# Optimization experiments

Measured on AMD Instinct MI355X. Metric: run time of the kernel, lower is better.

Reference implementation:

```python
import jax, jax.numpy as jnp
import numpy as np

B, N, FEAT, HID, OUT = 128, 64, 4, 256, 4
E = N * (N - 1)  # fully-connected graph, no self-loops


def _onehot_rel():
    # off-diagonal (recv, send) pairs, matching NRI's encode_onehot construction
    recv, send = np.where(~np.eye(N, dtype=bool))
    rel_rec = np.eye(N, dtype=np.float32)[recv]   # [E, N]
    rel_send = np.eye(N, dtype=np.float32)[send]  # [E, N]
    return jnp.asarray(rel_rec), jnp.asarray(rel_send)


def setup_inputs() -> dict:
    key = jax.random.key(0)
    ks = jax.random.split(key, 8)
    rel_rec, rel_send = _onehot_rel()

    def xavier(k, shape):
        fan_in, fan_out = shape
        lim = (6.0 / (fan_in + fan_out)) ** 0.5
        return jax.random.uniform(k, shape, jnp.float32, -lim, lim)

    return {
        "inputs": jax.random.normal(ks[0], (B, N, FEAT), jnp.float32),
        "edges": jax.random.normal(ks[1], (B, E, 2), jnp.float32),  # unused by forward (as in source)
        "rel_rec": rel_rec,
        "rel_send": rel_send,
        "W_msg1": xavier(ks[2], (2 * FEAT, HID)), "b_msg1": jnp.zeros((HID,), jnp.float32),
        "W_msg2": xavier(ks[3], (HID, HID)),      "b_msg2": jnp.zeros((HID,), jnp.float32),
        "W_out1": xavier(ks[4], (FEAT + HID, HID)), "b_out1": jnp.zeros((HID,), jnp.float32),
        "W_out2": xavier(ks[5], (HID, HID)),      "b_out2": jnp.zeros((HID,), jnp.float32),
        "W_out3": xavier(ks[6], (HID, OUT)),      "b_out3": jnp.zeros((OUT,), jnp.float32),
    }


def reference(inputs, edges, rel_rec, rel_send,
              W_msg1, b_msg1, W_msg2, b_msg2,
              W_out1, b_out1, W_out2, b_out2, W_out3, b_out3):
    x = inputs.reshape(inputs.shape[0], inputs.shape[1], -1)  # [B, N, F]
    # gather node features to edges via one-hot matmuls (faithful to source)
    receivers = jnp.einsum('en,bnf->bef', rel_rec, x)   # [B, E, F]
    senders = jnp.einsum('en,bnf->bef', rel_send, x)    # [B, E, F]
    pre_msg = jnp.concatenate([receivers, senders], axis=-1)  # [B, E, 2F]
    # edge MLP (dropout_prob = 0.0 -> identity)
    msg = jax.nn.relu(pre_msg @ W_msg1 + b_msg1)
    msg = jax.nn.relu(msg @ W_msg2 + b_msg2)            # [B, E, HID]
    # scatter-aggregate back to nodes via rel_rec^T
    agg_msg = jnp.einsum('en,beh->bnh', rel_rec, msg)   # [B, N, HID]
    out = jnp.concatenate([x, agg_msg], axis=-1)        # [B, N, F+HID]
    out = jax.nn.relu(out @ W_out1 + b_out1)
    out = jax.nn.relu(out @ W_out2 + b_out2)
    out = out @ W_out3 + b_out3                          # [B, N, 4]
    return out
```

## Files before the change

kernel.cpp:

```cpp
#include <hip/hip_runtime.h>
#include <cstddef>

typedef _Float16 f16_t;
typedef _Float16 f16x8 __attribute__((ext_vector_type(8)));
typedef float    f32x4 __attribute__((ext_vector_type(4)));

static constexpr int NN = 64;
static constexpr int FF = 4;
static constexpr int HH = 256;


__device__ inline void pack_frag(const float* __restrict__ src, f16_t* __restrict__ dst,
                                 int fid, int ksteps, int mode)
{
    if (fid >= ksteps * 1024) return;
    int lane = fid & 63;
    int nt   = (fid >> 6) & 15;
    int ks   = fid >> 10;
    int col  = nt * 16 + (lane & 15);
    int kb   = ks * 32 + (lane >> 4) * 8;
    #pragma unroll
    for (int j = 0; j < 8; ++j) {
        int k = kb + j;
        float v;
        if (mode == 0) {
            v = src[k * 256 + col];
        } else {
            if (k < 256)      v = src[(4 + k) * 256 + col];
            else if (k < 260) v = src[(k - 256) * 256 + col];
            else              v = 0.f;
        }
        dst[(size_t)fid * 8 + j] = (f16_t)v;
    }
}

__global__ void prep_all(const float* __restrict__ x,
                         const float* __restrict__ W_msg1,
                         const float* __restrict__ W_msg2,
                         const float* __restrict__ W_out1,
                         const float* __restrict__ W_out2,
                         f16_t* __restrict__ W2p, f16_t* __restrict__ W1op,
                         f16_t* __restrict__ W2op, f16_t* __restrict__ Vp)
{
    int bid = blockIdx.x, tid = threadIdx.x;
    if (bid < 32) {
        pack_frag(W_msg2, W2p, bid * 256 + tid, 8, 0);
    } else if (bid < 68) {
        pack_frag(W_out1, W1op, (bid - 32) * 256 + tid, 9, 1);
    } else if (bid < 100) {
        pack_frag(W_out2, W2op, (bid - 68) * 256 + tid, 8, 0);
    } else {
        int gid  = (bid - 100) * 256 + tid;
        int rown = gid >> 5;
        int h0   = (gid & 31) * 8;
        float4 xv = ((const float4*)x)[rown];
        f16x8 o;
        #pragma unroll
        for (int u = 0; u < 8; ++u) {
            float s = xv.x * W_msg1[4 * HH + h0 + u] + xv.y * W_msg1[5 * HH + h0 + u]
                    + xv.z * W_msg1[6 * HH + h0 + u] + xv.w * W_msg1[7 * HH + h0 + u];
            o[u] = (f16_t)s;
        }
        *(f16x8*)(Vp + (size_t)rown * HH + h0) = o;
    }
}

__global__ __launch_bounds__(512, 4) void edge_kernel(
    const float* __restrict__ x,
    const float* __restrict__ W1,
    const float* __restrict__ b1,
    const f16_t* __restrict__ Vp,
    const f16_t* __restrict__ W2p,
    const float* __restrict__ b2,
    f16_t* __restrict__ innode)
{
    __shared__ __align__(16) char h1[128 * 512];
    __shared__ __align__(16) f16_t Utab[2][256];

    const int tid  = threadIdx.x;
    const int lane = tid & 63;
    const int w    = tid >> 6;
    const int b    = blockIdx.x >> 5;
    const int pr   = blockIdx.x & 31;
    const int i0   = pr * 2, i1 = i0 + 1;

    {
        int rs   = tid >> 8;
        int h    = tid & 255;
        int node = rs ? i1 : i0;
        const float* xr = x + (b * NN + node) * FF;
        float s = b1[h] + xr[0] * W1[h] + xr[1] * W1[HH + h]
                        + xr[2] * W1[2 * HH + h] + xr[3] * W1[3 * HH + h];
        Utab[rs][h] = (f16_t)s;
    }
    if (tid < 64) {
        int node = (tid < 32) ? i0 : i1;
        int c = tid & 31;
        float v = (c < 4) ? x[(b * NN + node) * FF + c] : 0.f;
        innode[(size_t)(b * NN + node) * 288 + 256 + c] = (f16_t)v;
    }
    __syncthreads();

    {
        const int hb = tid & 31;
        const int rg = tid >> 5;
        const int h0 = hb * 8;
        const int recv = (rg < 8) ? i0 : i1;
        const f16x8 fz = {};
        f16x8 u8 = *(const f16x8*)&Utab[rg >> 3][h0];
        const int j0 = (rg & 7) * 8;
        const f16x8* vrow = (const f16x8*)(Vp + (size_t)(b * NN + j0) * HH + h0);
        #pragma unroll
        for (int k = 0; k < 8; ++k) {
            int r = rg * 8 + k;
            int j = j0 + k;
            f16x8 v8 = vrow[k * (HH / 8)];
            f16x8 hv = __builtin_elementwise_max(u8 + v8, fz);
            if (j == recv) hv = fz;
            *(f16x8*)(h1 + ((r * 512 + hb * 16) ^ ((r & 7) << 4))) = hv;
        }
    }
    __syncthreads();

    const int lm = lane & 15, lk = lane >> 4;
    const int mth = w >> 2;
    const int ntq = w & 3;

    float b2v[4];
    #pragma unroll
    for (int nt = 0; nt < 4; ++nt) b2v[nt] = b2[(ntq * 4 + nt) * 16 + lm];

    f32x4 acc[4][4];
    #pragma unroll
    for (int mt = 0; mt < 4; ++mt)
        #pragma unroll
        for (int nt = 0; nt < 4; ++nt)
            acc[mt][nt] = (f32x4){b2v[nt], b2v[nt], b2v[nt], b2v[nt]};

    #pragma unroll
    for (int ks = 0; ks < 8; ++ks) {
        f16x8 a[4];
        #pragma unroll
        for (int mt = 0; mt < 4; ++mt) {
            int r = (mth * 4 + mt) * 16 + lm;
            a[mt] = *(const f16x8*)(h1 + ((r * 512 + ks * 64 + lk * 16) ^ ((r & 7) << 4)));
        }
        #pragma unroll
        for (int nt = 0; nt < 4; ++nt) {
            f16x8 bb = *(const f16x8*)(W2p + (size_t)((ks * 16 + ntq * 4 + nt) * 64 + lane) * 8);
            #pragma unroll
            for (int mt = 0; mt < 4; ++mt)
                acc[mt][nt] = __builtin_amdgcn_mfma_f32_16x16x32_f16(a[mt], bb, acc[mt][nt], 0, 0, 0);
        }
    }

    const int recv = (mth == 0) ? i0 : i1;
    float agg[4] = {0, 0, 0, 0};
    #pragma unroll
    for (int mt = 0; mt < 4; ++mt)
        #pragma unroll
        for (int nt = 0; nt < 4; ++nt) {
            float s = fmaxf(acc[mt][nt][0], 0.f);
            s += fmaxf(acc[mt][nt][1], 0.f);
            s += fmaxf(acc[mt][nt][2], 0.f);
            s += fmaxf(acc[mt][nt][3], 0.f);
            agg[nt] += s;
        }
    #pragma unroll
    for (int nt = 0; nt < 4; ++nt) {
        agg[nt] += __shfl_xor(agg[nt], 16);
        agg[nt] += __shfl_xor(agg[nt], 32);
    }
    if (lane < 16) {
        #pragma unroll
        for (int nt = 0; nt < 4; ++nt) {
            int col = (ntq * 4 + nt) * 16 + lane;
            innode[(size_t)(b * NN + recv) * 288 + col] =
                (f16_t)(agg[nt] - fmaxf(b2v[nt], 0.f));
        }
    }
}

__global__ __launch_bounds__(512, 2) void node_kernel(
    const f16_t* __restrict__ innode,
    const f16_t* __restrict__ W1op,
    const float* __restrict__ bo1,
    const f16_t* __restrict__ W2op,
    const float* __restrict__ bo2,
    const float* __restrict__ W3,
    const float* __restrict__ bo3,
    float* __restrict__ out)
{
    __shared__ __align__(16) char bufA[32 * 640];
    __shared__ __align__(16) char bufB[32 * 512];
    __shared__ __align__(16) char bufC[32 * 528];

    const int tid  = threadIdx.x;
    const int lane = tid & 63;
    const int w    = tid >> 6;
    const int m0   = blockIdx.x * 32;
    const int lm   = lane & 15, lk = lane >> 4;
    const int mt   = w >> 2;
    const int ntq  = w & 3;

    for (int idx = tid; idx < 32 * 36; idx += 512) {
        int r = idx / 36, c = idx - r * 36;
        f16x8 v = *(const f16x8*)(innode + (size_t)(m0 + r) * 288 + c * 8);
        *(f16x8*)(bufA + ((r * 640 + c * 16) ^ ((r & 7) << 4))) = v;
    }
    __syncthreads();

    f32x4 acc1[4];
    #pragma unroll
    for (int nt = 0; nt < 4; ++nt) {
        float bias = bo1[(ntq * 4 + nt) * 16 + lm];
        acc1[nt] = (f32x4){bias, bias, bias, bias};
    }
    #pragma unroll
    for (int ks = 0; ks < 9; ++ks) {
        int r = mt * 16 + lm;
        f16x8 a = *(const f16x8*)(bufA + ((r * 640 + ks * 64 + lk * 16) ^ ((r & 7) << 4)));
        #pragma unroll
        for (int nt = 0; nt < 4; ++nt) {
            f16x8 bb = *(const f16x8*)(W1op + (size_t)((ks * 16 + ntq * 4 + nt) * 64 + lane) * 8);
            acc1[nt] = __builtin_amdgcn_mfma_f32_16x16x32_f16(a, bb, acc1[nt], 0, 0, 0);
        }
    }
    #pragma unroll
    for (int nt = 0; nt < 4; ++nt) {
        int col = (ntq * 4 + nt) * 16 + lm;
        #pragma unroll
        for (int j = 0; j < 4; ++j) {
            int row = mt * 16 + lk * 4 + j;
            float v = fmaxf(acc1[nt][j], 0.f);
            *(f16_t*)(bufB + ((row * 512 + col * 2) ^ ((row & 7) << 4))) = (f16_t)v;
        }
    }
    __syncthreads();

    f32x4 acc2[4];
    #pragma unroll
    for (int nt = 0; nt < 4; ++nt) {
        float bias = bo2[(ntq * 4 + nt) * 16 + lm];
        acc2[nt] = (f32x4){bias, bias, bias, bias};
    }
    #pragma unroll
    for (int ks = 0; ks < 8; ++ks) {
        int r = mt * 16 + lm;
        f16x8 a = *(const f16x8*)(bufB + ((r * 512 + ks * 64 + lk * 16) ^ ((r & 7) << 4)));
        #pragma unroll
        for (int nt = 0; nt < 4; ++nt) {
            f16x8 bb = *(const f16x8*)(W2op + (size_t)((ks * 16 + ntq * 4 + nt) * 64 + lane) * 8);
            acc2[nt] = __builtin_amdgcn_mfma_f32_16x16x32_f16(a, bb, acc2[nt], 0, 0, 0);
        }
    }
    f16_t* c16 = (f16_t*)bufC;
    #pragma unroll
    for (int nt = 0; nt < 4; ++nt) {
        int col = (ntq * 4 + nt) * 16 + lm;
        #pragma unroll
        for (int j = 0; j < 4; ++j) {
            int row = mt * 16 + lk * 4 + j;
            float v = fmaxf(acc2[nt][j], 0.f);
            c16[row * 264 + col] = (f16_t)v;
        }
    }
    __syncthreads();

    {
        int m = tid >> 4;
        int o = (tid >> 2) & 3;
        int q = tid & 3;
        const f16_t* crow = c16 + m * 264 + q * 64;
        float s = 0.f;
        int rot = (lane & 15) * 4;
        #pragma unroll 8
        for (int k = 0; k < 64; ++k) {
            int kk = (k + rot) & 63;
            s += (float)crow[kk] * W3[(q * 64 + kk) * 4 + o];
        }
        s += __shfl_xor(s, 1);
        s += __shfl_xor(s, 2);
        if (q == 0) out[(size_t)(m0 + m) * 4 + o] = s + bo3[o];
    }
}

extern "C" void kernel_launch(void* const* d_in, const int* in_sizes, int n_in,
                              void* d_out, int out_size, void* d_ws, size_t ws_size,
                              hipStream_t stream)
{
    (void)in_sizes; (void)n_in; (void)out_size; (void)ws_size;
    const float* x      = (const float*)d_in[0];
    const float* W_msg1 = (const float*)d_in[4];
    const float* b_msg1 = (const float*)d_in[5];
    const float* W_msg2 = (const float*)d_in[6];
    const float* b_msg2 = (const float*)d_in[7];
    const float* W_out1 = (const float*)d_in[8];
    const float* b_out1 = (const float*)d_in[9];
    const float* W_out2 = (const float*)d_in[10];
    const float* b_out2 = (const float*)d_in[11];
    const float* W_out3 = (const float*)d_in[12];
    const float* b_out3 = (const float*)d_in[13];
    float* out = (float*)d_out;

    char* ws = (char*)d_ws;
    f16_t* W2p    = (f16_t*)(ws + 0);
    f16_t* W1op   = (f16_t*)(ws + 131072);
    f16_t* W2op   = (f16_t*)(ws + 278528);
    f16_t* innode = (f16_t*)(ws + 409600);
    f16_t* Vp     = (f16_t*)(ws + 5128192);

    prep_all<<<1124, 256, 0, stream>>>(x, W_msg1, W_msg2, W_out1, W_out2,
                                       W2p, W1op, W2op, Vp);
    edge_kernel<<<4096, 512, 0, stream>>>(x, W_msg1, b_msg1, Vp, W2p, b_msg2, innode);
    node_kernel<<<256, 512, 0, stream>>>(innode, W1op, b_out1, W2op, b_out2,
                                         W_out3, b_out3, out);
}
```

Measured before the change: 96.97 us.

## Switch edge GEMM to 32x32x16 MFMA with per-wave column ownership

Repacks W_msg2 into 32x32x16 MFMA B fragments and rewrites the edge kernel's second GEMM so each of the 8 waves owns 32 output columns across all 128 edge rows, using four 32x32 accumulators. This replaces 16x16x32 MFMAs with a 2x4 wave grid, aiming to cut per-wave B-fragment loads and simplify the reduction to a single cross-half shuffle. The LDS swizzle becomes a full 5-bit XOR, and the self-loop zeroing moves out of the inner loop into one conditional store. Register pressure rises from the 64-float accumulators, which may affect occupancy under the (512,4) launch bound.

```diff
diff --git a/kernel.cpp b/kernel.cpp
--- a/kernel.cpp
+++ b/kernel.cpp
@@ -3,15 +3,16 @@
 
 typedef _Float16 f16_t;
 typedef _Float16 f16x8 __attribute__((ext_vector_type(8)));
-typedef float    f32x4 __attribute__((ext_vector_type(4)));
+typedef float    f32x4  __attribute__((ext_vector_type(4)));
+typedef float    f32x16 __attribute__((ext_vector_type(16)));
 
 static constexpr int NN = 64;
 static constexpr int FF = 4;
 static constexpr int HH = 256;
 
 
-__device__ inline void pack_frag(const float* __restrict__ src, f16_t* __restrict__ dst,
-                                 int fid, int ksteps, int mode)
+__device__ inline void pack_frag16(const float* __restrict__ src, f16_t* __restrict__ dst,
+                                   int fid, int ksteps, int mode)
 {
     if (fid >= ksteps * 1024) return;
     int lane = fid & 63;
@@ -34,6 +35,19 @@
     }
 }
 
+__device__ inline void pack_frag32(const float* __restrict__ src, f16_t* __restrict__ dst,
+                                   int fid)
+{
+    int lane = fid & 63;
+    int nt   = (fid >> 6) & 7;
+    int ks   = fid >> 9;
+    int col  = nt * 32 + (lane & 31);
+    int kb   = ks * 16 + (lane >> 5) * 8;
+    #pragma unroll
+    for (int j = 0; j < 8; ++j)
+        dst[(size_t)fid * 8 + j] = (f16_t)src[(kb + j) * 256 + col];
+}
+
 __global__ void prep_all(const float* __restrict__ x,
                          const float* __restrict__ W_msg1,
                          const float* __restrict__ W_msg2,
@@ -44,11 +58,11 @@
 {
     int bid = blockIdx.x, tid = threadIdx.x;
     if (bid < 32) {
-        pack_frag(W_msg2, W2p, bid * 256 + tid, 8, 0);
+        pack_frag32(W_msg2, W2p, bid * 256 + tid);
     } else if (bid < 68) {
-        pack_frag(W_out1, W1op, (bid - 32) * 256 + tid, 9, 1);
+        pack_frag16(W_out1, W1op, (bid - 32) * 256 + tid, 9, 1);
     } else if (bid < 100) {
-        pack_frag(W_out2, W2op, (bid - 68) * 256 + tid, 8, 0);
+        pack_frag16(W_out2, W2op, (bid - 68) * 256 + tid, 8, 0);
     } else {
         int gid  = (bid - 100) * 256 + tid;
         int rown = gid >> 5;
@@ -113,71 +127,55 @@
         #pragma unroll
         for (int k = 0; k < 8; ++k) {
             int r = rg * 8 + k;
-            int j = j0 + k;
             f16x8 v8 = vrow[k * (HH / 8)];
             f16x8 hv = __builtin_elementwise_max(u8 + v8, fz);
-            if (j == recv) hv = fz;
-            *(f16x8*)(h1 + ((r * 512 + hb * 16) ^ ((r & 7) << 4))) = hv;
-        }
-    }
-    __syncthreads();
-
-    const int lm = lane & 15, lk = lane >> 4;
-    const int mth = w >> 2;
-    const int ntq = w & 3;
-
-    float b2v[4];
-    #pragma unroll
-    for (int nt = 0; nt < 4; ++nt) b2v[nt] = b2[(ntq * 4 + nt) * 16 + lm];
-
-    f32x4 acc[4][4];
+            *(f16x8*)(h1 + r * 512 + (((hb ^ (r & 31)) & 31) << 4)) = hv;
+        }
+        if ((rg & 7) == (recv >> 3)) {
+            int k = recv & 7;
+            int r = rg * 8 + k;
+            *(f16x8*)(h1 + r * 512 + (((hb ^ (r & 31)) & 31) << 4)) = fz;
+        }
+    }
+    __syncthreads();
+
+    const int ln = lane & 31;
+    const int kh = lane >> 5;
+
+    const float b2v = b2[w * 32 + ln];
+    f32x16 acc[4];
     #pragma unroll
     for (int mt = 0; mt < 4; ++mt)
         #pragma unroll
-        for (int nt = 0; nt < 4; ++nt)
-            acc[mt][nt] = (f32x4){b2v[nt], b2v[nt], b2v[nt], b2v[nt]};
-
-    #pragma unroll
-    for (int ks = 0; ks < 8; ++ks) {
-        f16x8 a[4];
+        for (int e = 0; e < 16; ++e) acc[mt][e] = b2v;
+
+    #pragma unroll
+    for (int ks = 0; ks < 16; ++ks) {
+        f16x8 bb = *(const f16x8*)(W2p + (size_t)((ks * 8 + w) * 64 + lane) * 8);
         #pragma unroll
         for (int mt = 0; mt < 4; ++mt) {
-            int r = (mth * 4 + mt) * 16 + lm;
-            a[mt] = *(const f16x8*)(h1 + ((r * 512 + ks * 64 + lk * 16) ^ ((r & 7) << 4)));
-        }
-        #pragma unroll
-        for (int nt = 0; nt < 4; ++nt) {
-            f16x8 bb = *(const f16x8*)(W2p + (size_t)((ks * 16 + ntq * 4 + nt) * 64 + lane) * 8);
-            #pragma unroll
-            for (int mt = 0; mt < 4; ++mt)
-                acc[mt][nt] = __builtin_amdgcn_mfma_f32_16x16x32_f16(a[mt], bb, acc[mt][nt], 0, 0, 0);
-        }
-    }
-
-    const int recv = (mth == 0) ? i0 : i1;
-    float agg[4] = {0, 0, 0, 0};
-    #pragma unroll
-    for (int mt = 0; mt < 4; ++mt)
-        #pragma unroll
-        for (int nt = 0; nt < 4; ++nt) {
-            float s = fmaxf(acc[mt][nt][0], 0.f);
-            s += fmaxf(acc[mt][nt][1], 0.f);
-            s += fmaxf(acc[mt][nt][2], 0.f);
-            s += fmaxf(acc[mt][nt][3], 0.f);
-            agg[nt] += s;
-        }
-    #pragma unroll
-    for (int nt = 0; nt < 4; ++nt) {
-        agg[nt] += __shfl_xor(agg[nt], 16);
-        agg[nt] += __shfl_xor(agg[nt], 32);
-    }
-    if (lane < 16) {
-        #pragma unroll
-        for (int nt = 0; nt < 4; ++nt) {
-            int col = (ntq * 4 + nt) * 16 + lane;
-            innode[(size_t)(b * NN + recv) * 288 + col] =
-                (f16_t)(agg[nt] - fmaxf(b2v[nt], 0.f));
-        }
+            int row = mt * 32 + ln;
+            int c16 = (ks * 2 + kh) ^ (row & 31);
+            f16x8 a = *(const f16x8*)(h1 + row * 512 + (c16 << 4));
+            acc[mt] = __builtin_amdgcn_mfma_f32_32x32x16_f16(a, bb, acc[mt], 0, 0, 0);
+        }
+    }
+
+    float s0 = 0.f, s1 = 0.f;
+    #pragma unroll
+    for (int mt = 0; mt < 4; ++mt) {
+        float s = 0.f;
+        #pragma unroll
+        for (int e = 0; e < 16; ++e) s += fmaxf(acc[mt][e], 0.f);
+        if (mt < 2) s0 += s; else s1 += s;
+    }
+    s0 += __shfl_xor(s0, 32);
+    s1 += __shfl_xor(s1, 32);
+    if (lane < 32) {
+        float sub = fmaxf(b2v, 0.f);
+        int col = w * 32 + ln;
+        innode[(size_t)(b * NN + i0) * 288 + col] = (f16_t)(s0 - sub);
+        innode[(size_t)(b * NN + i1) * 288 + col] = (f16_t)(s1 - sub);
     }
 }
 
```

After: 100.7 us. +3.8%, slower.
